# Kernel optimization log

Hardware: AMD Instinct MI355X
Metric: run time of the kernel (lower is better)

Reference implementation:

```python
import jax, jax.numpy as jnp
import numpy as np

V, D, H, L, MAXS = 32000, 768, 12, 6, 2048
HD = D // H  # 64
FF = 4 * D
B, S = 8, 1024
EPS = 1e-5


def _make_pe():
    pos = np.arange(MAXS, dtype=np.float32)[:, None]
    div = np.exp(np.arange(0, D, 2, dtype=np.float32) * (-np.log(10000.0) / D))
    pe = np.zeros((MAXS, D), dtype=np.float32)
    pe[:, 0::2] = np.sin(pos * div)
    pe[:, 1::2] = np.cos(pos * div)
    return jnp.asarray(pe)


def setup_inputs() -> dict:
    key = jax.random.key(0)
    ks = jax.random.split(key, 16)
    sc = 0.02
    return {
        "tokens": jax.random.randint(ks[0], (B, S), 0, V),
        "k_mask": jnp.ones((B, S), dtype=jnp.int32),
        "emb": jax.random.normal(ks[1], (V, D), jnp.float32) * sc,
        "pe": _make_pe(),
        "ln1_s": jnp.ones((L, D), jnp.float32),
        "ln1_b": jnp.zeros((L, D), jnp.float32),
        "wq": jax.random.normal(ks[2], (L, H, D, HD), jnp.float32) * sc,
        "wk": jax.random.normal(ks[3], (L, H, D, HD), jnp.float32) * sc,
        "wv": jax.random.normal(ks[4], (L, H, D, HD), jnp.float32) * sc,
        "wo": jax.random.normal(ks[5], (L, D, D), jnp.float32) * sc,
        "ln2_s": jnp.ones((L, D), jnp.float32),
        "ln2_b": jnp.zeros((L, D), jnp.float32),
        "w1": jax.random.normal(ks[6], (L, D, FF), jnp.float32) * sc,
        "b1": jnp.zeros((L, FF), jnp.float32),
        "w2": jax.random.normal(ks[7], (L, FF, D), jnp.float32) * sc,
        "b2": jnp.zeros((L, D), jnp.float32),
    }


def _ln(x, s, b):
    m = jnp.mean(x, axis=-1, keepdims=True)
    v = jnp.var(x, axis=-1, keepdims=True)
    return (x - m) * jax.lax.rsqrt(v + EPS) * s + b


def _forward(tokens, k_mask, emb, pe, ln1_s, ln1_b, wq, wk, wv, wo,
             ln2_s, ln2_b, w1, b1, w2, b2):
    x = emb[tokens] + pe[None, :tokens.shape[1], :]  # [B,S,D]
    mask = (k_mask != 0)[:, None, None, :]  # [B,1,1,S]
    for l in range(L):
        xn = _ln(x, ln1_s[l], ln1_b[l])
        q = jnp.einsum('bsd,hde->bhse', xn, wq[l])
        k = jnp.einsum('bsd,hde->bhse', xn, wk[l])
        v = jnp.einsum('bsd,hde->bhse', xn, wv[l])
        scores = jnp.einsum('bhse,bhte->bhst', q, k) / (HD ** 0.5)
        scores = jnp.where(mask, scores, -jnp.inf)
        attn = jax.nn.softmax(scores, axis=-1)
        o = jnp.einsum('bhst,bhte->bhse', attn, v)  # [B,H,S,HD]
        o = o.transpose(0, 2, 1, 3).reshape(x.shape)  # concat heads -> [B,S,D]
        x = x + o @ wo[l]
        xn = _ln(x, ln2_s[l], ln2_b[l])
        h = jax.nn.gelu(xn @ w1[l] + b1[l], approximate=False)
        x = x + h @ w2[l] + b2[l]
    return x


def reference(tokens, k_mask, emb, pe, ln1_s, ln1_b, wq, wk, wv, wo,
              ln2_s, ln2_b, w1, b1, w2, b2):
    return _forward(tokens, k_mask, emb, pe, ln1_s, ln1_b, wq, wk, wv, wo,
                    ln2_s, ln2_b, w1, b1, w2, b2)
```

## Files before the change

kernel.cpp:

```cpp
#include <hip/hip_runtime.h>
#include <math.h>

typedef unsigned short u16;
typedef unsigned int u32;
typedef __attribute__((ext_vector_type(8))) __bf16 bf16x8;
typedef __attribute__((ext_vector_type(4))) float f32x4;
typedef __attribute__((ext_vector_type(8))) unsigned short ushort8v;
typedef __attribute__((ext_vector_type(4))) float float4v;
typedef __attribute__((ext_vector_type(4))) unsigned short u16x4;

typedef const __attribute__((address_space(1))) void gvoid_t;
typedef __attribute__((address_space(3))) void lvoid_t;

#define MFMA(a, b, c) __builtin_amdgcn_mfma_f32_16x16x32_bf16((a), (b), (c), 0, 0, 0)

__device__ __forceinline__ u16 f2bf(float f) {
  __bf16 h = (__bf16)f;
  return __builtin_bit_cast(u16, h);
}

__device__ __forceinline__ void stage64(const u16* g, int ldg, u16* lds, int rows, int tid) {
  int w = tid >> 6, l = tid & 63;
  int lr = l >> 3;
  int cb = (l & 7) << 4;
  for (int it = 0; it < rows; it += 32) {
    int rbase = it + w * 8;
    int r = rbase + lr;
    int scb = cb ^ ((r & 7) << 4);
    const char* gp = (const char*)(g + (size_t)r * ldg) + scb;
    char* lp = (char*)lds + (size_t)rbase * 128;
    __builtin_amdgcn_global_load_lds((gvoid_t*)gp, (lvoid_t*)lp, 16, 0, 0);
  }
}

__device__ __forceinline__ bf16x8 ldsfrag(const u16* base, int row, int e0) {
  int boff = row * 128 + (((e0) << 1) ^ ((row & 7) << 4));
  return *(const bf16x8*)((const char*)base + boff);
}

__global__ void embed_kernel(const int* __restrict__ tok, const float* __restrict__ emb,
                             const float* __restrict__ pe, float* __restrict__ xf) {
  int row = blockIdx.x;
  int tid = threadIdx.x;
  int t = tok[row];
  int spos = row & 1023;
  float4v e = ((const float4v*)(emb + (size_t)t * 768))[tid];
  float4v p = ((const float4v*)(pe + (size_t)spos * 768))[tid];
  float4v r;
  r.x = e.x + p.x; r.y = e.y + p.y; r.z = e.z + p.z; r.w = e.w + p.w;
  ((float4v*)(xf + (size_t)row * 768))[tid] = r;
}

__global__ void ln_kernel(const float* __restrict__ x, const float* __restrict__ sc,
                          const float* __restrict__ bi, u16* __restrict__ out) {
  int row = blockIdx.x;
  int tid = threadIdx.x;
  float4v v = ((const float4v*)(x + (size_t)row * 768))[tid];
  float s = v.x + v.y + v.z + v.w;
  float s2 = v.x * v.x + v.y * v.y + v.z * v.z + v.w * v.w;
  #pragma unroll
  for (int off = 32; off >= 1; off >>= 1) {
    s += __shfl_down(s, off);
    s2 += __shfl_down(s2, off);
  }
  __shared__ float red[8];
  if ((tid & 63) == 0) { red[tid >> 6] = s; red[4 + (tid >> 6)] = s2; }
  __syncthreads();
  float S = red[0] + red[1] + red[2];
  float S2 = red[4] + red[5] + red[6];
  float m = S * (1.0f / 768.0f);
  float var = S2 * (1.0f / 768.0f) - m * m;
  float rs = rsqrtf(var + 1e-5f);
  float4v sv = ((const float4v*)sc)[tid];
  float4v bv = ((const float4v*)bi)[tid];
  u16x4 ov;
  ov.x = f2bf((v.x - m) * rs * sv.x + bv.x);
  ov.y = f2bf((v.y - m) * rs * sv.y + bv.y);
  ov.z = f2bf((v.z - m) * rs * sv.z + bv.z);
  ov.w = f2bf((v.w - m) * rs * sv.w + bv.w);
  *(u16x4*)(out + (size_t)row * 768 + tid * 4) = ov;
}

__global__ void convT_kernel(const float* __restrict__ src, u16* __restrict__ dst,
                             int N, int K, long long sz, long long dz) {
  src += (size_t)blockIdx.z * sz;
  dst += (size_t)blockIdx.z * dz;
  __shared__ float t[32][33];
  int n0 = blockIdx.x * 32, k0 = blockIdx.y * 32;
  int tid = threadIdx.x;
  int tx = tid & 31, ty = tid >> 5;
  for (int r = ty; r < 32; r += 8) t[r][tx] = src[(size_t)(k0 + r) * N + n0 + tx];
  __syncthreads();
  for (int r = ty; r < 32; r += 8) dst[(size_t)(n0 + r) * K + k0 + tx] = f2bf(t[tx][r]);
}

__global__ void convqkvT_kernel(const float* __restrict__ wq, const float* __restrict__ wk,
                                const float* __restrict__ wv, u16* __restrict__ dst,
                                long long wz, long long dz) {
  __shared__ float t[32][33];
  int n0 = blockIdx.x * 32, k0 = blockIdx.y * 32;
  int which = n0 / 768;
  int r0 = n0 % 768;
  int h = r0 >> 6, e0 = r0 & 63;
  const float* src = which == 0 ? wq : (which == 1 ? wk : wv);
  src += (size_t)blockIdx.z * wz;
  dst += (size_t)blockIdx.z * dz;
  int tid = threadIdx.x;
  int tx = tid & 31, ty = tid >> 5;
  for (int r = ty; r < 32; r += 8) t[r][tx] = src[(size_t)(h * 768 + k0 + r) * 64 + e0 + tx];
  __syncthreads();
  for (int r = ty; r < 32; r += 8) dst[(size_t)(n0 + r) * 768 + k0 + tx] = f2bf(t[tx][r]);
}

__global__ void transpose_v_kernel(const u16* __restrict__ v, u16* __restrict__ vt) {
  __shared__ u16 t[64][72];
  int bh = blockIdx.x, sc = blockIdx.y;
  int tid = threadIdx.x;
  const u16* src = v + ((size_t)bh * 1024 + sc * 64) * 64;
  int sl = tid >> 2, e0 = (tid & 3) * 16;
  ushort8v a = *(const ushort8v*)(src + (size_t)sl * 64 + e0);
  ushort8v b = *(const ushort8v*)(src + (size_t)sl * 64 + e0 + 8);
  #pragma unroll
  for (int j = 0; j < 8; ++j) t[sl][e0 + j] = a[j];
  #pragma unroll
  for (int j = 0; j < 8; ++j) t[sl][e0 + 8 + j] = b[j];
  __syncthreads();
  int e = tid >> 2, s0 = (tid & 3) * 16;
  ushort8v o0, o1;
  #pragma unroll
  for (int j = 0; j < 8; ++j) o0[j] = t[s0 + j][e];
  #pragma unroll
  for (int j = 0; j < 8; ++j) o1[j] = t[s0 + 8 + j][e];
  u16* dst = vt + ((size_t)bh * 64 + e) * 1024 + sc * 64 + s0;
  *(ushort8v*)dst = o0;
  *(ushort8v*)(dst + 8) = o1;
}

template <int MODE, int NK>
__global__ __launch_bounds__(256) void gemm128(
    const u16* __restrict__ A, int lda, const u16* __restrict__ Wt, int ldb, int kOuter,
    float* __restrict__ xf, u16* __restrict__ outb, const float* __restrict__ bias,
    u16* __restrict__ qb, u16* __restrict__ kb, u16* __restrict__ vb) {
  __shared__ alignas(16) u16 As[128 * 64];
  __shared__ alignas(16) u16 Bs[128 * 64];
  int tid = threadIdx.x, lane = tid & 63, w = tid >> 6;
  int wm = w >> 1, wn = w & 1;
  int m0 = blockIdx.x * 128, n0 = blockIdx.y * 128;
  f32x4 acc[4][4] = {};
  int lr = lane >> 3;
  int cb = (lane & 7) << 4;
  int sws = cb ^ (lr << 4);
  const char* pA = (const char*)(A + (size_t)m0 * lda) + (size_t)(w * 8 + lr) * (lda * 2) + sws;
  const char* pB = (const char*)(Wt + (size_t)n0 * ldb) + (size_t)(w * 8 + lr) * (ldb * 2) + sws;
  char* dA = (char*)As + w * 1024;
  char* dB = (char*)Bs + w * 1024;
  int arow = wm * 64 + (lane & 15);
  int brow = wn * 64 + (lane & 15);
  int e0 = (lane >> 4) * 8;
  for (int c = 0; c < kOuter; ++c) {
    #pragma unroll
    for (int kt = 0; kt < NK; ++kt) {
      __syncthreads();
      #pragma unroll
      for (int i = 0; i < 4; ++i) {
        __builtin_amdgcn_global_load_lds((gvoid_t*)(pA + (size_t)i * 32 * (lda * 2)),
                                         (lvoid_t*)(dA + i * 4096), 16, 0, 0);
        __builtin_amdgcn_global_load_lds((gvoid_t*)(pB + (size_t)i * 32 * (ldb * 2)),
                                         (lvoid_t*)(dB + i * 4096), 16, 0, 0);
      }
      pA += 128; pB += 128;
      __syncthreads();
      #pragma unroll
      for (int kk = 0; kk < 2; ++kk) {
        bf16x8 af[4], bfr[4];
        #pragma unroll
        for (int mt = 0; mt < 4; ++mt) af[mt] = ldsfrag(As, arow + mt * 16, kk * 32 + e0);
        #pragma unroll
        for (int nt = 0; nt < 4; ++nt) bfr[nt] = ldsfrag(Bs, brow + nt * 16, kk * 32 + e0);
        #pragma unroll
        for (int mt = 0; mt < 4; ++mt)
          #pragma unroll
          for (int nt = 0; nt < 4; ++nt)
            acc[mt][nt] = MFMA(af[mt], bfr[nt], acc[mt][nt]);
      }
    }
  }
  int rbase = m0 + wm * 64 + ((lane >> 4) << 2);
  int cbase = n0 + wn * 64 + (lane & 15);
  if constexpr (MODE == 0) {
    int which = n0 / 768;
    u16* dstb = which == 0 ? qb : (which == 1 ? kb : vb);
    int cloc = cbase - which * 768;
    #pragma unroll
    for (int mt = 0; mt < 4; ++mt) {
      #pragma unroll
      for (int nt = 0; nt < 4; ++nt) {
        int rr = cloc + nt * 16;
        int h = rr >> 6, e = rr & 63;
        #pragma unroll
        for (int reg = 0; reg < 4; ++reg) {
          int row = rbase + mt * 16 + reg;
          int b = row >> 10, s = row & 1023;
          dstb[((size_t)(b * 12 + h) * 1024 + s) * 64 + e] = f2bf(acc[mt][nt][reg]);
        }
      }
    }
  } else if constexpr (MODE == 2) {
    #pragma unroll
    for (int mt = 0; mt < 4; ++mt) {
      #pragma unroll
      for (int nt = 0; nt < 4; ++nt) {
        int col = cbase + nt * 16;
        float bb = bias[col];
        #pragma unroll
        for (int reg = 0; reg < 4; ++reg) {
          int row = rbase + mt * 16 + reg;
          float t = acc[mt][nt][reg] + bb;
          float u = t * fmaf(t * t, 0.044715f, 1.0f);
          float ex = __builtin_amdgcn_exp2f(u * -2.3022156f);
          float g = t * __builtin_amdgcn_rcpf(1.0f + ex);
          outb[(size_t)row * 3072 + col] = f2bf(g);
        }
      }
    }
  } else {
    #pragma unroll
    for (int mt = 0; mt < 4; ++mt) {
      #pragma unroll
      for (int nt = 0; nt < 4; ++nt) {
        int col = cbase + nt * 16;
        float bb = (MODE == 3) ? bias[col] : 0.0f;
        #pragma unroll
        for (int reg = 0; reg < 4; ++reg) {
          int row = rbase + mt * 16 + reg;
          xf[(size_t)row * 768 + col] += acc[mt][nt][reg] + bb;
        }
      }
    }
  }
}

__global__ __launch_bounds__(256) void flash64(
    const u16* __restrict__ q, const u16* __restrict__ k, const u16* __restrict__ vt,
    const int* __restrict__ kmask, u16* __restrict__ o) {
  __shared__ alignas(16) u16 Qs[64 * 64];
  __shared__ alignas(16) u16 Ks[2][64 * 64];
  __shared__ alignas(16) u16 Vs[2][64 * 64];
  __shared__ alignas(16) u16 Ps[64 * 64];
  int tid = threadIdx.x, lane = tid & 63, w = tid >> 6;
  int lc = lane & 15;
  int bh = blockIdx.x, q0 = blockIdx.y * 64;
  int b = bh / 12, h = bh % 12;

  stage64(q + ((size_t)bh * 1024 + q0) * 64, 64, Qs, 64, tid);
  __syncthreads();
  int qrow = w * 16 + lc;
  int e0 = (lane >> 4) * 8;
  bf16x8 aq0 = ldsfrag(Qs, qrow, e0);
  bf16x8 aq1 = ldsfrag(Qs, qrow, 32 + e0);

  bf16x8 ones;
  #pragma unroll
  for (int j = 0; j < 8; ++j) ones[j] = (__bf16)1.0f;

  f32x4 oacc[4] = {};
  f32x4 lacc = {};
  const float SCL = 0.125f * 1.44269504f;
  const float SH = -3.0f * 1.44269504f;
  int prow_base = w * 16 + ((lane >> 4) << 2);

  stage64(k + (size_t)bh * 1024 * 64, 64, Ks[0], 64, tid);
  stage64(vt + (size_t)bh * 64 * 1024, 1024, Vs[0], 64, tid);

  for (int kt = 0; kt < 16; ++kt) {
    asm volatile("s_waitcnt vmcnt(0)" ::: "memory");
    __builtin_amdgcn_sched_barrier(0);
    __builtin_amdgcn_s_barrier();
    __builtin_amdgcn_sched_barrier(0);
    const u16* Kc = Ks[kt & 1];
    const u16* Vc = Vs[kt & 1];

    f32x4 sacc[4] = {};
    #pragma unroll
    for (int nt = 0; nt < 4; ++nt) {
      bf16x8 bk = ldsfrag(Kc, nt * 16 + lc, e0);
      sacc[nt] = MFMA(aq0, bk, sacc[nt]);
    }
    #pragma unroll
    for (int nt = 0; nt < 4; ++nt) {
      bf16x8 bk = ldsfrag(Kc, nt * 16 + lc, 32 + e0);
      sacc[nt] = MFMA(aq1, bk, sacc[nt]);
    }

    if (kt + 1 < 16) {
      stage64(k + ((size_t)bh * 1024 + (kt + 1) * 64) * 64, 64, Ks[(kt + 1) & 1], 64, tid);
      stage64(vt + (size_t)bh * 64 * 1024 + (kt + 1) * 64, 1024, Vs[(kt + 1) & 1], 64, tid);
    }

    #pragma unroll
    for (int nt = 0; nt < 4; ++nt) {
      int c = nt * 16 + lc;
      float mk = kmask[b * 1024 + kt * 64 + c] ? SH : -1e30f;
      #pragma unroll
      for (int r = 0; r < 4; ++r) {
        float p = __builtin_amdgcn_exp2f(fmaf(sacc[nt][r], SCL, mk));
        int prow = prow_base + r;
        int boff = prow * 128 + ((c << 1) ^ ((prow & 7) << 4));
        *(u16*)((char*)Ps + boff) = f2bf(p);
      }
    }

    bf16x8 ap0 = ldsfrag(Ps, qrow, e0);
    bf16x8 ap1 = ldsfrag(Ps, qrow, 32 + e0);
    lacc = MFMA(ap0, ones, lacc);
    lacc = MFMA(ap1, ones, lacc);
    #pragma unroll
    for (int et = 0; et < 4; ++et) {
      bf16x8 bv = ldsfrag(Vc, et * 16 + lc, e0);
      oacc[et] = MFMA(ap0, bv, oacc[et]);
    }
    #pragma unroll
    for (int et = 0; et < 4; ++et) {
      bf16x8 bv = ldsfrag(Vc, et * 16 + lc, 32 + e0);
      oacc[et] = MFMA(ap1, bv, oacc[et]);
    }
  }

  float rl[4];
  #pragma unroll
  for (int r = 0; r < 4; ++r) rl[r] = __builtin_amdgcn_rcpf(lacc[r]);
  int orow_base = q0 + prow_base;
  #pragma unroll
  for (int et = 0; et < 4; ++et) {
    int e = et * 16 + lc;
    #pragma unroll
    for (int r = 0; r < 4; ++r) {
      int row = orow_base + r;
      o[((size_t)(b * 1024 + row)) * 768 + h * 64 + e] = f2bf(oacc[et][r] * rl[r]);
    }
  }
}

__global__ void copy_kernel(const float* __restrict__ src, float* __restrict__ dst) {
  size_t i = (size_t)blockIdx.x * blockDim.x + threadIdx.x;
  ((float4v*)dst)[i] = ((const float4v*)src)[i];
}

extern "C" void kernel_launch(void* const* d_in, const int* in_sizes, int n_in,
                              void* d_out, int out_size, void* d_ws, size_t ws_size,
                              hipStream_t stream) {
  const int* tokens = (const int*)d_in[0];
  const int* kmask = (const int*)d_in[1];
  const float* emb = (const float*)d_in[2];
  const float* pe = (const float*)d_in[3];
  const float* ln1_s = (const float*)d_in[4];
  const float* ln1_b = (const float*)d_in[5];
  const float* wq = (const float*)d_in[6];
  const float* wk = (const float*)d_in[7];
  const float* wv = (const float*)d_in[8];
  const float* wo = (const float*)d_in[9];
  const float* ln2_s = (const float*)d_in[10];
  const float* ln2_b = (const float*)d_in[11];
  const float* w1 = (const float*)d_in[12];
  const float* b1 = (const float*)d_in[13];
  const float* w2 = (const float*)d_in[14];
  const float* b2 = (const float*)d_in[15];

  char* ws = (char*)d_ws;
  float* xf = (float*)ws;
  u16* xn   = (u16*)(ws + 25165824);
  u16* qb   = (u16*)(ws + 37748736);
  u16* kb   = (u16*)(ws + 50331648);
  u16* vb   = (u16*)(ws + 62914560);
  u16* vtb  = (u16*)(ws + 75497472);
  u16* ob   = (u16*)(ws + 88080384);
  u16* ffh  = (u16*)(ws + 100663296);

  const size_t SZ_QKV = (size_t)2304 * 768;
  const size_t SZ_O   = (size_t)768 * 768;
  const size_t SZ_F1  = (size_t)3072 * 768;
  const size_t SZ_F2  = (size_t)768 * 3072;
  const size_t NEED = 150994944 + 2 * 6 * (SZ_QKV + SZ_O + SZ_F1 + SZ_F2);
  bool pre = ws_size >= NEED;
  int nz = pre ? 6 : 1;
  u16* wqkvt = (u16*)(ws + 150994944);
  u16* wot   = wqkvt + (size_t)nz * SZ_QKV;
  u16* w1t   = wot + (size_t)nz * SZ_O;
  u16* w2t   = w1t + (size_t)nz * SZ_F1;

  embed_kernel<<<8192, 192, 0, stream>>>(tokens, emb, pe, xf);

  if (pre) {
    convqkvT_kernel<<<dim3(72, 24, 6), 256, 0, stream>>>(wq, wk, wv, wqkvt, 589824LL, (long long)SZ_QKV);
    convT_kernel<<<dim3(24, 24, 6), 256, 0, stream>>>(wo, wot, 768, 768, 589824LL, (long long)SZ_O);
    convT_kernel<<<dim3(96, 24, 6), 256, 0, stream>>>(w1, w1t, 3072, 768, 2359296LL, (long long)SZ_F1);
    convT_kernel<<<dim3(24, 96, 6), 256, 0, stream>>>(w2, w2t, 768, 3072, 2359296LL, (long long)SZ_F2);
  }

  for (int l = 0; l < 6; ++l) {
    size_t woff_qkv = (size_t)l * 12 * 768 * 64;
    size_t woff_o = (size_t)l * 768 * 768;
    size_t woff_ff = (size_t)l * 768 * 3072;
    const u16* wt_qkv_l = wqkvt + (pre ? (size_t)l * SZ_QKV : 0);
    const u16* wt_o_l   = wot   + (pre ? (size_t)l * SZ_O   : 0);
    const u16* wt_1_l   = w1t   + (pre ? (size_t)l * SZ_F1  : 0);
    const u16* wt_2_l   = w2t   + (pre ? (size_t)l * SZ_F2  : 0);

    if (!pre) {
      convqkvT_kernel<<<dim3(72, 24, 1), 256, 0, stream>>>(wq + woff_qkv, wk + woff_qkv, wv + woff_qkv, (u16*)wt_qkv_l, 0LL, 0LL);
      convT_kernel<<<dim3(24, 24, 1), 256, 0, stream>>>(wo + woff_o, (u16*)wt_o_l, 768, 768, 0LL, 0LL);
      convT_kernel<<<dim3(96, 24, 1), 256, 0, stream>>>(w1 + woff_ff, (u16*)wt_1_l, 3072, 768, 0LL, 0LL);
      convT_kernel<<<dim3(24, 96, 1), 256, 0, stream>>>(w2 + woff_ff, (u16*)wt_2_l, 768, 3072, 0LL, 0LL);
    }

    ln_kernel<<<8192, 192, 0, stream>>>(xf, ln1_s + l * 768, ln1_b + l * 768, xn);
    gemm128<0, 6><<<dim3(64, 18, 1), 256, 0, stream>>>(xn, 768, wt_qkv_l, 768, 2, nullptr, nullptr, nullptr, qb, kb, vb);
    transpose_v_kernel<<<dim3(96, 16), 256, 0, stream>>>(vb, vtb);
    flash64<<<dim3(96, 16), 256, 0, stream>>>(qb, kb, vtb, kmask, ob);
    gemm128<1, 6><<<dim3(64, 6, 1), 256, 0, stream>>>(ob, 768, wt_o_l, 768, 2, xf, nullptr, nullptr, nullptr, nullptr, nullptr);
    ln_kernel<<<8192, 192, 0, stream>>>(xf, ln2_s + l * 768, ln2_b + l * 768, xn);
    gemm128<2, 6><<<dim3(64, 24, 1), 256, 0, stream>>>(xn, 768, wt_1_l, 768, 2, nullptr, ffh, b1 + l * 3072, nullptr, nullptr, nullptr);
    gemm128<3, 6><<<dim3(64, 6, 1), 256, 0, stream>>>(ffh, 3072, wt_2_l, 3072, 8, xf, nullptr, b2 + l * 768, nullptr, nullptr, nullptr);
  }

  copy_kernel<<<6144, 256, 0, stream>>>(xf, (float*)d_out);
}
```

Baseline: 1.594 ms.

## Replace GEMM with triple-buffered K=32 LDS ring and smaller M tiles for N=768 GEMMs

Rewrites the bf16 GEMM to use a three-slot LDS ring with K-steps of 32. Global-to-LDS loads for step t+2 are issued while step t computes, and explicit vmcnt waits plus a single barrier per iteration replace the two syncthreads per 64-wide K step. The output-projection and FFN2 GEMMs switch to 64-row M tiles, doubling their grid to improve CU occupancy on the narrow N=768 outputs. This trades more iterations and barriers with less MFMA work per step for overlap of loads and compute, and relies on hand-counted vmcnt values being correct.

```diff
diff --git a/kernel.cpp b/kernel.cpp
--- a/kernel.cpp
+++ b/kernel.cpp
@@ -36,6 +36,22 @@
 __device__ __forceinline__ bf16x8 ldsfrag(const u16* base, int row, int e0) {
   int boff = row * 128 + (((e0) << 1) ^ ((row & 7) << 4));
   return *(const bf16x8*)((const char*)base + boff);
+}
+
+template <int ROWS>
+__device__ __forceinline__ void stage32(const u16* g, int ldg, char* dst, int tid) {
+  #pragma unroll
+  for (int i = 0; i < ROWS / 64; ++i) {
+    int row = i * 64 + (tid >> 2);
+    int slot = (tid & 3) ^ ((row >> 1) & 3);
+    const char* gp = (const char*)(g + (size_t)row * ldg) + (slot << 4);
+    char* lp = dst + i * 4096 + (tid >> 6) * 1024;
+    __builtin_amdgcn_global_load_lds((gvoid_t*)gp, (lvoid_t*)lp, 16, 0, 0);
+  }
+}
+
+__device__ __forceinline__ bf16x8 ringfrag(const char* base, int r, int t) {
+  return *(const bf16x8*)(base + r * 64 + ((t ^ ((r >> 1) & 3)) << 4));
 }
 
 __global__ void embed_kernel(const int* __restrict__ tok, const float* __restrict__ emb,
@@ -136,65 +152,85 @@
   *(ushort8v*)(dst + 8) = o1;
 }
 
-template <int MODE, int NK>
-__global__ __launch_bounds__(256) void gemm128(
-    const u16* __restrict__ A, int lda, const u16* __restrict__ Wt, int ldb, int kOuter,
+template <int MODE, int BM>
+__global__ __launch_bounds__(256) void gemm2p(
+    const u16* __restrict__ A, int lda, const u16* __restrict__ Wt, int ldb, int niter,
     float* __restrict__ xf, u16* __restrict__ outb, const float* __restrict__ bias,
     u16* __restrict__ qb, u16* __restrict__ kb, u16* __restrict__ vb) {
-  __shared__ alignas(16) u16 As[128 * 64];
-  __shared__ alignas(16) u16 Bs[128 * 64];
+  constexpr int ASZ = BM * 64;
+  constexpr int SLOT = ASZ + 8192;
+  constexpr int LPT = BM / 64 + 2;
+  constexpr int MT = (BM == 128) ? 4 : 4;
+  constexpr int NT = (BM == 128) ? 4 : 2;
+  __shared__ alignas(16) char lds[3 * SLOT];
   int tid = threadIdx.x, lane = tid & 63, w = tid >> 6;
-  int wm = w >> 1, wn = w & 1;
-  int m0 = blockIdx.x * 128, n0 = blockIdx.y * 128;
-  f32x4 acc[4][4] = {};
-  int lr = lane >> 3;
-  int cb = (lane & 7) << 4;
-  int sws = cb ^ (lr << 4);
-  const char* pA = (const char*)(A + (size_t)m0 * lda) + (size_t)(w * 8 + lr) * (lda * 2) + sws;
-  const char* pB = (const char*)(Wt + (size_t)n0 * ldb) + (size_t)(w * 8 + lr) * (ldb * 2) + sws;
-  char* dA = (char*)As + w * 1024;
-  char* dB = (char*)Bs + w * 1024;
-  int arow = wm * 64 + (lane & 15);
-  int brow = wn * 64 + (lane & 15);
-  int e0 = (lane >> 4) * 8;
-  for (int c = 0; c < kOuter; ++c) {
-    #pragma unroll
-    for (int kt = 0; kt < NK; ++kt) {
-      __syncthreads();
+  int lc = lane & 15, tq = lane >> 4;
+  int m0 = blockIdx.x * BM, n0 = blockIdx.y * 128;
+  const u16* Ag = A + (size_t)m0 * lda;
+  const u16* Bg = Wt + (size_t)n0 * ldb;
+  f32x4 acc[MT][NT] = {};
+  int wm = (BM == 128) ? (w >> 1) : 0;
+  int wn = (BM == 128) ? (w & 1) : w;
+  int nband = (BM == 128) ? 64 : 32;
+
+  stage32<BM>(Ag, lda, lds, tid);
+  stage32<128>(Bg, ldb, lds + ASZ, tid);
+  stage32<BM>(Ag + 32, lda, lds + SLOT, tid);
+  stage32<128>(Bg + 32, ldb, lds + SLOT + ASZ, tid);
+  if (LPT == 4) asm volatile("s_waitcnt vmcnt(4)" ::: "memory");
+  else          asm volatile("s_waitcnt vmcnt(3)" ::: "memory");
+  __builtin_amdgcn_sched_barrier(0);
+  __builtin_amdgcn_s_barrier();
+  __builtin_amdgcn_sched_barrier(0);
+
+  int cur = 0;
+  for (int t = 0; t < niter; ++t) {
+    const char* sa = lds + cur * SLOT;
+    const char* sb = sa + ASZ;
+    if (t + 2 < niter) {
+      int stg = cur - 1; if (stg < 0) stg = 2;
+      char* d = lds + stg * SLOT;
+      stage32<BM>(Ag + (t + 2) * 32, lda, d, tid);
+      stage32<128>(Bg + (t + 2) * 32, ldb, d + ASZ, tid);
+    }
+    bf16x8 af[MT], bfr[NT];
+    #pragma unroll
+    for (int mt = 0; mt < MT; ++mt) af[mt] = ringfrag(sa, wm * 64 + mt * 16 + lc, tq);
+    #pragma unroll
+    for (int nt = 0; nt < NT; ++nt) bfr[nt] = ringfrag(sb, wn * nband + nt * 16 + lc, tq);
+    asm volatile("s_waitcnt lgkmcnt(0)" ::: "memory");
+    __builtin_amdgcn_sched_barrier(0);
+    __builtin_amdgcn_s_setprio(1);
+    #pragma unroll
+    for (int mt = 0; mt < MT; ++mt)
       #pragma unroll
-      for (int i = 0; i < 4; ++i) {
-        __builtin_amdgcn_global_load_lds((gvoid_t*)(pA + (size_t)i * 32 * (lda * 2)),
-                                         (lvoid_t*)(dA + i * 4096), 16, 0, 0);
-        __builtin_amdgcn_global_load_lds((gvoid_t*)(pB + (size_t)i * 32 * (ldb * 2)),
-                                         (lvoid_t*)(dB + i * 4096), 16, 0, 0);
+      for (int nt = 0; nt < NT; ++nt)
+        acc[mt][nt] = MFMA(af[mt], bfr[nt], acc[mt][nt]);
+    __builtin_amdgcn_s_setprio(0);
+    if (t + 1 < niter) {
+      if (t + 2 < niter) {
+        if (LPT == 4) asm volatile("s_waitcnt vmcnt(4)" ::: "memory");
+        else          asm volatile("s_waitcnt vmcnt(3)" ::: "memory");
+      } else {
+        asm volatile("s_waitcnt vmcnt(0)" ::: "memory");
       }
-      pA += 128; pB += 128;
-      __syncthreads();
-      #pragma unroll
-      for (int kk = 0; kk < 2; ++kk) {
-        bf16x8 af[4], bfr[4];
-        #pragma unroll
-        for (int mt = 0; mt < 4; ++mt) af[mt] = ldsfrag(As, arow + mt * 16, kk * 32 + e0);
-        #pragma unroll
-        for (int nt = 0; nt < 4; ++nt) bfr[nt] = ldsfrag(Bs, brow + nt * 16, kk * 32 + e0);
-        #pragma unroll
-        for (int mt = 0; mt < 4; ++mt)
-          #pragma unroll
-          for (int nt = 0; nt < 4; ++nt)
-            acc[mt][nt] = MFMA(af[mt], bfr[nt], acc[mt][nt]);
-      }
-    }
-  }
-  int rbase = m0 + wm * 64 + ((lane >> 4) << 2);
-  int cbase = n0 + wn * 64 + (lane & 15);
+      __builtin_amdgcn_sched_barrier(0);
+      __builtin_amdgcn_s_barrier();
+      __builtin_amdgcn_sched_barrier(0);
+    }
+    cur = (cur == 2) ? 0 : cur + 1;
+  }
+
+  int rbase = m0 + wm * 64 + (tq << 2);
+  int cbase = n0 + wn * nband + lc;
   if constexpr (MODE == 0) {
     int which = n0 / 768;
     u16* dstb = which == 0 ? qb : (which == 1 ? kb : vb);
     int cloc = cbase - which * 768;
     #pragma unroll
-    for (int mt = 0; mt < 4; ++mt) {
+    for (int mt = 0; mt < MT; ++mt) {
       #pragma unroll
-      for (int nt = 0; nt < 4; ++nt) {
+      for (int nt = 0; nt < NT; ++nt) {
         int rr = cloc + nt * 16;
         int h = rr >> 6, e = rr & 63;
         #pragma unroll
@@ -207,9 +243,9 @@
     }
   } else if constexpr (MODE == 2) {
     #pragma unroll
-    for (int mt = 0; mt < 4; ++mt) {
+    for (int mt = 0; mt < MT; ++mt) {
       #pragma unroll
-      for (int nt = 0; nt < 4; ++nt) {
+      for (int nt = 0; nt < NT; ++nt) {
         int col = cbase + nt * 16;
         float bb = bias[col];
         #pragma unroll
@@ -225,9 +261,9 @@
     }
   } else {
     #pragma unroll
-    for (int mt = 0; mt < 4; ++mt) {
+    for (int mt = 0; mt < MT; ++mt) {
       #pragma unroll
-      for (int nt = 0; nt < 4; ++nt) {
+      for (int nt = 0; nt < NT; ++nt) {
         int col = cbase + nt * 16;
         float bb = (MODE == 3) ? bias[col] : 0.0f;
         #pragma unroll
@@ -414,13 +450,13 @@
     }
 
     ln_kernel<<<8192, 192, 0, stream>>>(xf, ln1_s + l * 768, ln1_b + l * 768, xn);
-    gemm128<0, 6><<<dim3(64, 18, 1), 256, 0, stream>>>(xn, 768, wt_qkv_l, 768, 2, nullptr, nullptr, nullptr, qb, kb, vb);
+    gemm2p<0, 128><<<dim3(64, 18), 256, 0, stream>>>(xn, 768, wt_qkv_l, 768, 24, nullptr, nullptr, nullptr, qb, kb, vb);
     transpose_v_kernel<<<dim3(96, 16), 256, 0, stream>>>(vb, vtb);
     flash64<<<dim3(96, 16), 256, 0, stream>>>(qb, kb, vtb, kmask, ob);
-    gemm128<1, 6><<<dim3(64, 6, 1), 256, 0, stream>>>(ob, 768, wt_o_l, 768, 2, xf, nullptr, nullptr, nullptr, nullptr, nullptr);
+    gemm2p<1, 64><<<dim3(128, 6), 256, 0, stream>>>(ob, 768, wt_o_l, 768, 24, xf, nullptr, nullptr, nullptr, nullptr, nullptr);
     ln_kernel<<<8192, 192, 0, stream>>>(xf, ln2_s + l * 768, ln2_b + l * 768, xn);
-    gemm128<2, 6><<<dim3(64, 24, 1), 256, 0, stream>>>(xn, 768, wt_1_l, 768, 2, nullptr, ffh, b1 + l * 3072, nullptr, nullptr, nullptr);
-    gemm128<3, 6><<<dim3(64, 6, 1), 256, 0, stream>>>(ffh, 3072, wt_2_l, 3072, 8, xf, nullptr, b2 + l * 768, nullptr, nullptr, nullptr);
+    gemm2p<2, 128><<<dim3(64, 24), 256, 0, stream>>>(xn, 768, wt_1_l, 768, 24, nullptr, ffh, b1 + l * 3072, nullptr, nullptr, nullptr);
+    gemm2p<3, 64><<<dim3(128, 6), 256, 0, stream>>>(ffh, 3072, wt_2_l, 3072, 96, xf, nullptr, b2 + l * 768, nullptr, nullptr, nullptr);
   }
 
   copy_kernel<<<6144, 256, 0, stream>>>(xf, (float*)d_out);
```

New measurement: 1.645 ms. +3.2%, slower.
